# Performance work log

Measured on AMD Instinct MI355X. Metric: run time of the kernel, lower is better.

Reference implementation:

```python
import jax, jax.numpy as jnp
import numpy as np

B, T, D_IN, H, C = 256, 2048, 64, 32, 16
RHO, SPARSITY = 0.9, 0.1


def _reservoir(rng, n):
    # uniform(-1,1), scale to spectral radius RHO, then sparsify (same order as torch code)
    W = rng.uniform(-1.0, 1.0, (n, n)).astype(np.float32)
    W *= RHO / np.max(np.abs(np.linalg.eigvals(W)))
    W *= (rng.random((n, n)) < SPARSITY).astype(np.float32)
    return jnp.asarray(W)


def _linear(rng, fan_in, fan_out):
    bound = 1.0 / np.sqrt(fan_in)
    W = rng.uniform(-bound, bound, (fan_out, fan_in)).astype(np.float32)
    b = rng.uniform(-bound, bound, (fan_out,)).astype(np.float32)
    return jnp.asarray(W), jnp.asarray(b)


def setup_inputs() -> dict:
    key = jax.random.key(0)
    rng = np.random.default_rng(0)
    x = jax.random.normal(key, (B, T, D_IN), dtype=jnp.float32)
    # frozen encoder input / reservoir weights (uniform(-1,1) weights, default-init biases)
    W_in = jnp.asarray(rng.uniform(-1.0, 1.0, (H, D_IN)).astype(np.float32))
    b_in = jnp.asarray(rng.uniform(-1 / np.sqrt(D_IN), 1 / np.sqrt(D_IN), (H,)).astype(np.float32))
    W_res_enc = _reservoir(rng, H)
    b_res_enc = jnp.asarray(rng.uniform(-1 / np.sqrt(H), 1 / np.sqrt(H), (H,)).astype(np.float32))
    W_code, b_code = _linear(rng, H, C)
    W_co, b_co = _linear(rng, C, H)
    W_res_dec = _reservoir(rng, H)
    b_res_dec = jnp.asarray(rng.uniform(-1 / np.sqrt(H), 1 / np.sqrt(H), (H,)).astype(np.float32))
    W_ro, b_ro = _linear(rng, H, D_IN)
    return dict(x=x, W_in=W_in, b_in=b_in, W_res_enc=W_res_enc, b_res_enc=b_res_enc,
                W_code=W_code, b_code=b_code, W_co=W_co, b_co=b_co,
                W_res_dec=W_res_dec, b_res_dec=b_res_dec, W_ro=W_ro, b_ro=b_ro)


def reference(x, W_in, b_in, W_res_enc, b_res_enc, W_code, b_code, W_co, b_co,
              W_res_dec, b_res_dec, W_ro, b_ro):
    Bs = x.shape[0]
    h0 = jnp.zeros((Bs, W_res_enc.shape[0]), dtype=x.dtype)
    # precompute input projection for all timesteps: [T, B, H]
    u_enc = jnp.swapaxes(jnp.einsum('btd,hd->bth', x, W_in) + b_in, 0, 1)

    def enc_step(h, u):
        h = jnp.tanh(u + h @ W_res_enc.T + b_res_enc)
        return h, h

    _, enc = jax.lax.scan(enc_step, h0, u_enc)
    enc = jnp.swapaxes(enc, 0, 1)                      # [B, T, H]

    z = enc @ W_code.T + b_code                        # [B, T, C]
    h_dec_in = z @ W_co.T + b_co                       # [B, T, H]

    def dec_step(h, u):
        h = jnp.tanh(u + h @ W_res_dec.T + b_res_dec)
        return h, h

    _, dec = jax.lax.scan(dec_step, h0, jnp.swapaxes(h_dec_in, 0, 1))
    dec = jnp.swapaxes(dec, 0, 1)                      # [B, T, H]
    return dec @ W_ro.T + b_ro                         # [B, T, D_IN]
```

## Files before the change

### kernel.cpp

```cpp
#include <hip/hip_runtime.h>
#include <math.h>

#define B_    256
#define T_    2048
#define DIN   64
#define H_    32
#define C_    16

#define CHUNK 256
#define WARM  96
#define NCHUNK (T_ / CHUNK)

#define OFF_WCOMB 0u
#define OFF_BCOMB 4096u
#define OFF_U     (1u << 20)

__device__ __forceinline__ float fast_tanh(float x) {
    float e2 = __expf(x + x);
    return 1.0f - 2.0f * __builtin_amdgcn_rcpf(e2 + 1.0f);
}

__global__ __launch_bounds__(1024) void prep_kernel(
        const float* __restrict__ W_code, const float* __restrict__ b_code,
        const float* __restrict__ W_co,   const float* __restrict__ b_co,
        float* __restrict__ W_comb, float* __restrict__ b_comb) {
    int t = threadIdx.x;
    int i = t >> 5, j = t & 31;
    float s = 0.0f;
#pragma unroll
    for (int c = 0; c < C_; ++c)
        s += W_co[i * C_ + c] * W_code[c * H_ + j];
    W_comb[i * H_ + j] = s;
    if (t < H_) {
        float sb = b_co[t];
#pragma unroll
        for (int c = 0; c < C_; ++c)
            sb += W_co[t * C_ + c] * b_code[c];
        b_comb[t] = sb;
    }
}

__global__ __launch_bounds__(256) void inproj_kernel(
        const float* __restrict__ x, const float* __restrict__ W_in,
        const float* __restrict__ b_in, float* __restrict__ u) {
    __shared__ __align__(16) float4 lx[128 * 16];

    int tid  = threadIdx.x;
    int w    = tid >> 6;
    int lane = tid & 63;
    int i    = lane & 31;
    int par  = lane >> 5;

    float Wr[DIN];
    {
        const float4* wi4 = reinterpret_cast<const float4*>(W_in + i * DIN);
#pragma unroll
        for (int q = 0; q < DIN / 4; ++q) {
            float4 v = wi4[q];
            Wr[4*q+0] = v.x; Wr[4*q+1] = v.y; Wr[4*q+2] = v.z; Wr[4*q+3] = v.w;
        }
    }
    float bi = b_in[i];

    long row_base = (long)blockIdx.x * 128;
    const float4* xg = reinterpret_cast<const float4*>(x) + row_base * 16;

#pragma unroll
    for (int k = 0; k < 8; ++k)
        lx[tid + 256 * k] = xg[tid + 256 * k];
    __syncthreads();

#pragma unroll
    for (int g = 0; g < 4; ++g) {
        int r0 = w * 32 + g * 8 + par;
        float acc0 = 0.f, acc1 = 0.f, acc2 = 0.f, acc3 = 0.f;
#pragma unroll
        for (int k4 = 0; k4 < 16; ++k4) {
            float4 wv = { Wr[4*k4+0], Wr[4*k4+1], Wr[4*k4+2], Wr[4*k4+3] };
            float4 x0 = lx[(r0 + 0) * 16 + k4];
            float4 x1 = lx[(r0 + 2) * 16 + k4];
            float4 x2 = lx[(r0 + 4) * 16 + k4];
            float4 x3 = lx[(r0 + 6) * 16 + k4];
            acc0 += x0.x * wv.x + x0.y * wv.y + x0.z * wv.z + x0.w * wv.w;
            acc1 += x1.x * wv.x + x1.y * wv.y + x1.z * wv.z + x1.w * wv.w;
            acc2 += x2.x * wv.x + x2.y * wv.y + x2.z * wv.z + x2.w * wv.w;
            acc3 += x3.x * wv.x + x3.y * wv.y + x3.z * wv.z + x3.w * wv.w;
        }
        long rg = row_base + r0;
        u[(rg + 0) * H_ + i] = acc0 + bi;
        u[(rg + 2) * H_ + i] = acc1 + bi;
        u[(rg + 4) * H_ + i] = acc2 + bi;
        u[(rg + 6) * H_ + i] = acc3 + bi;
    }
}

__global__ __launch_bounds__(64, 1) void scan_kernel(
        const float* __restrict__ u,
        const float* __restrict__ W_res_enc, const float* __restrict__ b_res_enc,
        const float* __restrict__ W_res_dec, const float* __restrict__ b_res_dec,
        const float* __restrict__ W_comb,    const float* __restrict__ b_comb,
        const float* __restrict__ W_ro,      const float* __restrict__ b_ro,
        float* __restrict__ out) {
    int lane = threadIdx.x;
    int i = lane & 31;
    int half = lane >> 5;
    int b  = ((blockIdx.x & 127) << 1) | half;
    int c  = blockIdx.x >> 7;
    int t0 = c * CHUNK;
    int tstart = (c == 0) ? 0 : (t0 - WARM);
    int tend = t0 + CHUNK;

    float We[H_], Wc[H_], Wd[H_], Wo0[H_], Wo1[H_];
    {
        const float4* we4 = reinterpret_cast<const float4*>(W_res_enc + i * H_);
        const float4* wc4 = reinterpret_cast<const float4*>(W_comb + i * H_);
        const float4* wd4 = reinterpret_cast<const float4*>(W_res_dec + i * H_);
        const float4* wo0 = reinterpret_cast<const float4*>(W_ro + (2 * i) * H_);
        const float4* wo1 = reinterpret_cast<const float4*>(W_ro + (2 * i + 1) * H_);
#pragma unroll
        for (int q = 0; q < H_ / 4; ++q) {
            float4 a = we4[q], bq = wc4[q], d = wd4[q], o0 = wo0[q], o1 = wo1[q];
            We[4*q+0]=a.x;  We[4*q+1]=a.y;  We[4*q+2]=a.z;  We[4*q+3]=a.w;
            Wc[4*q+0]=bq.x; Wc[4*q+1]=bq.y; Wc[4*q+2]=bq.z; Wc[4*q+3]=bq.w;
            Wd[4*q+0]=d.x;  Wd[4*q+1]=d.y;  Wd[4*q+2]=d.z;  Wd[4*q+3]=d.w;
            Wo0[4*q+0]=o0.x;Wo0[4*q+1]=o0.y;Wo0[4*q+2]=o0.z;Wo0[4*q+3]=o0.w;
            Wo1[4*q+0]=o1.x;Wo1[4*q+1]=o1.y;Wo1[4*q+2]=o1.z;Wo1[4*q+3]=o1.w;
        }
    }
    float be = b_res_enc[i], bc = b_comb[i], bd = b_res_dec[i];
    float bo0 = b_ro[2 * i], bo1 = b_ro[2 * i + 1];

    float henc[H_], hdec[H_];
#pragma unroll
    for (int j = 0; j < H_; ++j) { henc[j] = 0.0f; hdec[j] = 0.0f; }

    __shared__ __align__(16) float lhe[2][H_];
    __shared__ __align__(16) float lhd[2][H_];

    const float* ub = u + ((long)b * T_) * H_ + i;
    float*       ob = out + ((long)b * T_) * DIN + 2 * i;

    float ucur = ub[(long)tstart * H_];
    for (int t = tstart; t < tend; ++t) {
        float unext = 0.0f;
        if (t + 1 < tend) unext = ub[(long)(t + 1) * H_];

        float a0 = ucur + be, a1 = 0.f, a2 = 0.f, a3 = 0.f;
#pragma unroll
        for (int j = 0; j < H_; j += 4) {
            a0 += We[j+0] * henc[j+0];
            a1 += We[j+1] * henc[j+1];
            a2 += We[j+2] * henc[j+2];
            a3 += We[j+3] * henc[j+3];
        }
        float a = fast_tanh((a0 + a1) + (a2 + a3));

        lhe[half][i] = a;
#pragma unroll
        for (int q = 0; q < H_ / 4; ++q) {
            float4 v = *reinterpret_cast<const float4*>(&lhe[half][4 * q]);
            henc[4*q+0] = v.x; henc[4*q+1] = v.y;
            henc[4*q+2] = v.z; henc[4*q+3] = v.w;
        }

        float g0 = bc + bd, g1 = 0.f, g2 = 0.f, g3 = 0.f;
#pragma unroll
        for (int j = 0; j < H_; j += 4) {
            g0 += Wc[j+0] * henc[j+0];
            g1 += Wc[j+1] * henc[j+1];
            g2 += Wc[j+2] * henc[j+2];
            g3 += Wc[j+3] * henc[j+3];
        }
        float d0 = 0.f, d1 = 0.f, d2 = 0.f, d3 = 0.f;
#pragma unroll
        for (int j = 0; j < H_; j += 4) {
            d0 += Wd[j+0] * hdec[j+0];
            d1 += Wd[j+1] * hdec[j+1];
            d2 += Wd[j+2] * hdec[j+2];
            d3 += Wd[j+3] * hdec[j+3];
        }
        float d = fast_tanh(((g0 + g1) + (g2 + g3)) + ((d0 + d1) + (d2 + d3)));

        lhd[half][i] = d;
#pragma unroll
        for (int q = 0; q < H_ / 4; ++q) {
            float4 v = *reinterpret_cast<const float4*>(&lhd[half][4 * q]);
            hdec[4*q+0] = v.x; hdec[4*q+1] = v.y;
            hdec[4*q+2] = v.z; hdec[4*q+3] = v.w;
        }

        if (t >= t0) {
            float s00 = bo0, s01 = 0.f, s10 = bo1, s11 = 0.f;
#pragma unroll
            for (int j = 0; j < H_; j += 2) {
                s00 += Wo0[j]     * hdec[j];
                s01 += Wo0[j + 1] * hdec[j + 1];
                s10 += Wo1[j]     * hdec[j];
                s11 += Wo1[j + 1] * hdec[j + 1];
            }
            float2 o = make_float2(s00 + s01, s10 + s11);
            *reinterpret_cast<float2*>(ob + (long)t * DIN) = o;
        }
        ucur = unext;
    }
}

extern "C" void kernel_launch(void* const* d_in, const int* in_sizes, int n_in,
                              void* d_out, int out_size, void* d_ws, size_t ws_size,
                              hipStream_t stream) {
    const float* x         = (const float*)d_in[0];
    const float* W_in      = (const float*)d_in[1];
    const float* b_in      = (const float*)d_in[2];
    const float* W_res_enc = (const float*)d_in[3];
    const float* b_res_enc = (const float*)d_in[4];
    const float* W_code    = (const float*)d_in[5];
    const float* b_code    = (const float*)d_in[6];
    const float* W_co      = (const float*)d_in[7];
    const float* b_co      = (const float*)d_in[8];
    const float* W_res_dec = (const float*)d_in[9];
    const float* b_res_dec = (const float*)d_in[10];
    const float* W_ro      = (const float*)d_in[11];
    const float* b_ro      = (const float*)d_in[12];
    float* out = (float*)d_out;

    char* ws = (char*)d_ws;
    float* W_comb = (float*)(ws + OFF_WCOMB);
    float* b_comb = (float*)(ws + OFF_BCOMB);
    float* u      = (float*)(ws + OFF_U);

    prep_kernel<<<1, 1024, 0, stream>>>(W_code, b_code, W_co, b_co, W_comb, b_comb);
    inproj_kernel<<<(B_ * T_) / 128, 256, 0, stream>>>(x, W_in, b_in, u);
    scan_kernel<<<(B_ / 2) * NCHUNK, 64, 0, stream>>>(u, W_res_enc, b_res_enc,
                                                      W_res_dec, b_res_dec,
                                                      W_comb, b_comb, W_ro, b_ro, out);
}
```

Baseline: 508.0 us.

## Split readout into separate kernel, shrink scan chunks, reorder scan step

Moves the W_ro readout out of the recurrent scan into its own GEMV kernel, so the scan writes decoder states to workspace instead of computing outputs inline. Chunk size drops to 128 with a 64-step warmup, doubling the number of scan blocks, and launch bounds now allow two blocks per CU. The loop is reordered so the decoder recurrence product overlaps the encoder LDS exchange. The input projection reads rows directly from global memory without an LDS stage. The shorter warmup risks a larger truncation error, and the extra pass over decoder states adds memory traffic.

```diff
diff --git a/kernel.cpp b/kernel.cpp
--- a/kernel.cpp
+++ b/kernel.cpp
@@ -7,13 +7,14 @@
 #define H_    32
 #define C_    16
 
-#define CHUNK 256
-#define WARM  96
+#define CHUNK 128
+#define WARM  64
 #define NCHUNK (T_ / CHUNK)
 
 #define OFF_WCOMB 0u
 #define OFF_BCOMB 4096u
 #define OFF_U     (1u << 20)
+#define OFF_DEC   ((1u << 20) + (64u << 20))
 
 __device__ __forceinline__ float fast_tanh(float x) {
     float e2 = __expf(x + x);
@@ -40,67 +41,49 @@
     }
 }
 
-__global__ __launch_bounds__(256) void inproj_kernel(
+__global__ __launch_bounds__(256, 3) void inproj_kernel(
         const float* __restrict__ x, const float* __restrict__ W_in,
         const float* __restrict__ b_in, float* __restrict__ u) {
-    __shared__ __align__(16) float4 lx[128 * 16];
-
     int tid  = threadIdx.x;
-    int w    = tid >> 6;
-    int lane = tid & 63;
-    int i    = lane & 31;
-    int par  = lane >> 5;
-
-    float Wr[DIN];
+    int wave = tid >> 6;
+    int l    = tid & 63;
+    int d    = l & 31;
+    int par  = l >> 5;
+
+    float W[DIN];
     {
-        const float4* wi4 = reinterpret_cast<const float4*>(W_in + i * DIN);
+        const float4* w4 = reinterpret_cast<const float4*>(W_in + d * DIN);
 #pragma unroll
         for (int q = 0; q < DIN / 4; ++q) {
-            float4 v = wi4[q];
-            Wr[4*q+0] = v.x; Wr[4*q+1] = v.y; Wr[4*q+2] = v.z; Wr[4*q+3] = v.w;
-        }
-    }
-    float bi = b_in[i];
-
-    long row_base = (long)blockIdx.x * 128;
-    const float4* xg = reinterpret_cast<const float4*>(x) + row_base * 16;
-
-#pragma unroll
-    for (int k = 0; k < 8; ++k)
-        lx[tid + 256 * k] = xg[tid + 256 * k];
-    __syncthreads();
-
-#pragma unroll
-    for (int g = 0; g < 4; ++g) {
-        int r0 = w * 32 + g * 8 + par;
-        float acc0 = 0.f, acc1 = 0.f, acc2 = 0.f, acc3 = 0.f;
-#pragma unroll
-        for (int k4 = 0; k4 < 16; ++k4) {
-            float4 wv = { Wr[4*k4+0], Wr[4*k4+1], Wr[4*k4+2], Wr[4*k4+3] };
-            float4 x0 = lx[(r0 + 0) * 16 + k4];
-            float4 x1 = lx[(r0 + 2) * 16 + k4];
-            float4 x2 = lx[(r0 + 4) * 16 + k4];
-            float4 x3 = lx[(r0 + 6) * 16 + k4];
-            acc0 += x0.x * wv.x + x0.y * wv.y + x0.z * wv.z + x0.w * wv.w;
-            acc1 += x1.x * wv.x + x1.y * wv.y + x1.z * wv.z + x1.w * wv.w;
-            acc2 += x2.x * wv.x + x2.y * wv.y + x2.z * wv.z + x2.w * wv.w;
-            acc3 += x3.x * wv.x + x3.y * wv.y + x3.z * wv.z + x3.w * wv.w;
-        }
-        long rg = row_base + r0;
-        u[(rg + 0) * H_ + i] = acc0 + bi;
-        u[(rg + 2) * H_ + i] = acc1 + bi;
-        u[(rg + 4) * H_ + i] = acc2 + bi;
-        u[(rg + 6) * H_ + i] = acc3 + bi;
-    }
-}
-
-__global__ __launch_bounds__(64, 1) void scan_kernel(
+            float4 v = w4[q];
+            W[4*q+0] = v.x; W[4*q+1] = v.y; W[4*q+2] = v.z; W[4*q+3] = v.w;
+        }
+    }
+    float bi = b_in[d];
+
+    long base = ((long)blockIdx.x * 4 + wave) * 64;
+    for (int it = 0; it < 32; ++it) {
+        long row = base + 2 * it + par;
+        const float4* xr = reinterpret_cast<const float4*>(x + row * DIN);
+        float a0 = bi, a1 = 0.f, a2 = 0.f, a3 = 0.f;
+#pragma unroll
+        for (int k = 0; k < DIN / 4; ++k) {
+            float4 v = xr[k];
+            a0 += v.x * W[4*k+0];
+            a1 += v.y * W[4*k+1];
+            a2 += v.z * W[4*k+2];
+            a3 += v.w * W[4*k+3];
+        }
+        u[row * H_ + d] = (a0 + a1) + (a2 + a3);
+    }
+}
+
+__global__ __launch_bounds__(64, 2) void scan_kernel(
         const float* __restrict__ u,
         const float* __restrict__ W_res_enc, const float* __restrict__ b_res_enc,
         const float* __restrict__ W_res_dec, const float* __restrict__ b_res_dec,
         const float* __restrict__ W_comb,    const float* __restrict__ b_comb,
-        const float* __restrict__ W_ro,      const float* __restrict__ b_ro,
-        float* __restrict__ out) {
+        float* __restrict__ dec) {
     int lane = threadIdx.x;
     int i = lane & 31;
     int half = lane >> 5;
@@ -110,98 +93,130 @@
     int tstart = (c == 0) ? 0 : (t0 - WARM);
     int tend = t0 + CHUNK;
 
-    float We[H_], Wc[H_], Wd[H_], Wo0[H_], Wo1[H_];
+    float We[H_], Wc[H_], Wd[H_];
     {
         const float4* we4 = reinterpret_cast<const float4*>(W_res_enc + i * H_);
         const float4* wc4 = reinterpret_cast<const float4*>(W_comb + i * H_);
         const float4* wd4 = reinterpret_cast<const float4*>(W_res_dec + i * H_);
-        const float4* wo0 = reinterpret_cast<const float4*>(W_ro + (2 * i) * H_);
-        const float4* wo1 = reinterpret_cast<const float4*>(W_ro + (2 * i + 1) * H_);
-#pragma unroll
-        for (int q = 0; q < H_ / 4; ++q) {
-            float4 a = we4[q], bq = wc4[q], d = wd4[q], o0 = wo0[q], o1 = wo1[q];
+#pragma unroll
+        for (int q = 0; q < H_ / 4; ++q) {
+            float4 a = we4[q], bq = wc4[q], dv = wd4[q];
             We[4*q+0]=a.x;  We[4*q+1]=a.y;  We[4*q+2]=a.z;  We[4*q+3]=a.w;
             Wc[4*q+0]=bq.x; Wc[4*q+1]=bq.y; Wc[4*q+2]=bq.z; Wc[4*q+3]=bq.w;
-            Wd[4*q+0]=d.x;  Wd[4*q+1]=d.y;  Wd[4*q+2]=d.z;  Wd[4*q+3]=d.w;
-            Wo0[4*q+0]=o0.x;Wo0[4*q+1]=o0.y;Wo0[4*q+2]=o0.z;Wo0[4*q+3]=o0.w;
-            Wo1[4*q+0]=o1.x;Wo1[4*q+1]=o1.y;Wo1[4*q+2]=o1.z;Wo1[4*q+3]=o1.w;
-        }
-    }
-    float be = b_res_enc[i], bc = b_comb[i], bd = b_res_dec[i];
-    float bo0 = b_ro[2 * i], bo1 = b_ro[2 * i + 1];
-
-    float henc[H_], hdec[H_];
-#pragma unroll
-    for (int j = 0; j < H_; ++j) { henc[j] = 0.0f; hdec[j] = 0.0f; }
+            Wd[4*q+0]=dv.x; Wd[4*q+1]=dv.y; Wd[4*q+2]=dv.z; Wd[4*q+3]=dv.w;
+        }
+    }
+    float be = b_res_enc[i];
+    float bcd = b_comb[i] + b_res_dec[i];
+
+    float he[H_], hd[H_];
+#pragma unroll
+    for (int j = 0; j < H_; ++j) { he[j] = 0.0f; hd[j] = 0.0f; }
 
     __shared__ __align__(16) float lhe[2][H_];
     __shared__ __align__(16) float lhd[2][H_];
 
     const float* ub = u + ((long)b * T_) * H_ + i;
-    float*       ob = out + ((long)b * T_) * DIN + 2 * i;
+    float*       db = dec + ((long)b * T_) * H_ + i;
+
+    float4 hdr[H_ / 4];
+#pragma unroll
+    for (int q = 0; q < H_ / 4; ++q) hdr[q] = make_float4(0.f, 0.f, 0.f, 0.f);
 
     float ucur = ub[(long)tstart * H_];
     for (int t = tstart; t < tend; ++t) {
+        float a0 = ucur + be, a1 = 0.f, a2 = 0.f, a3 = 0.f;
+#pragma unroll
+        for (int j = 0; j < H_; j += 4) {
+            a0 += We[j+0] * he[j+0];
+            a1 += We[j+1] * he[j+1];
+            a2 += We[j+2] * he[j+2];
+            a3 += We[j+3] * he[j+3];
+        }
+        float a = fast_tanh((a0 + a1) + (a2 + a3));
+
+        lhe[half][i] = a;
+        float4 her[H_ / 4];
+#pragma unroll
+        for (int q = 0; q < H_ / 4; ++q)
+            her[q] = *reinterpret_cast<const float4*>(&lhe[half][4 * q]);
+
+#pragma unroll
+        for (int q = 0; q < H_ / 4; ++q) {
+            hd[4*q+0] = hdr[q].x; hd[4*q+1] = hdr[q].y;
+            hd[4*q+2] = hdr[q].z; hd[4*q+3] = hdr[q].w;
+        }
+        float d0 = bcd, d1 = 0.f, d2 = 0.f, d3 = 0.f;
+#pragma unroll
+        for (int j = 0; j < H_; j += 4) {
+            d0 += Wd[j+0] * hd[j+0];
+            d1 += Wd[j+1] * hd[j+1];
+            d2 += Wd[j+2] * hd[j+2];
+            d3 += Wd[j+3] * hd[j+3];
+        }
+
         float unext = 0.0f;
         if (t + 1 < tend) unext = ub[(long)(t + 1) * H_];
 
-        float a0 = ucur + be, a1 = 0.f, a2 = 0.f, a3 = 0.f;
+#pragma unroll
+        for (int q = 0; q < H_ / 4; ++q) {
+            he[4*q+0] = her[q].x; he[4*q+1] = her[q].y;
+            he[4*q+2] = her[q].z; he[4*q+3] = her[q].w;
+        }
+
+        float g0 = 0.f, g1 = 0.f, g2 = 0.f, g3 = 0.f;
 #pragma unroll
         for (int j = 0; j < H_; j += 4) {
-            a0 += We[j+0] * henc[j+0];
-            a1 += We[j+1] * henc[j+1];
-            a2 += We[j+2] * henc[j+2];
-            a3 += We[j+3] * henc[j+3];
-        }
-        float a = fast_tanh((a0 + a1) + (a2 + a3));
-
-        lhe[half][i] = a;
-#pragma unroll
-        for (int q = 0; q < H_ / 4; ++q) {
-            float4 v = *reinterpret_cast<const float4*>(&lhe[half][4 * q]);
-            henc[4*q+0] = v.x; henc[4*q+1] = v.y;
-            henc[4*q+2] = v.z; henc[4*q+3] = v.w;
-        }
-
-        float g0 = bc + bd, g1 = 0.f, g2 = 0.f, g3 = 0.f;
-#pragma unroll
-        for (int j = 0; j < H_; j += 4) {
-            g0 += Wc[j+0] * henc[j+0];
-            g1 += Wc[j+1] * henc[j+1];
-            g2 += Wc[j+2] * henc[j+2];
-            g3 += Wc[j+3] * henc[j+3];
-        }
-        float d0 = 0.f, d1 = 0.f, d2 = 0.f, d3 = 0.f;
-#pragma unroll
-        for (int j = 0; j < H_; j += 4) {
-            d0 += Wd[j+0] * hdec[j+0];
-            d1 += Wd[j+1] * hdec[j+1];
-            d2 += Wd[j+2] * hdec[j+2];
-            d3 += Wd[j+3] * hdec[j+3];
+            g0 += Wc[j+0] * he[j+0];
+            g1 += Wc[j+1] * he[j+1];
+            g2 += Wc[j+2] * he[j+2];
+            g3 += Wc[j+3] * he[j+3];
         }
         float d = fast_tanh(((g0 + g1) + (g2 + g3)) + ((d0 + d1) + (d2 + d3)));
 
+        if (t >= t0) db[(long)t * H_] = d;
+
         lhd[half][i] = d;
 #pragma unroll
-        for (int q = 0; q < H_ / 4; ++q) {
-            float4 v = *reinterpret_cast<const float4*>(&lhd[half][4 * q]);
-            hdec[4*q+0] = v.x; hdec[4*q+1] = v.y;
-            hdec[4*q+2] = v.z; hdec[4*q+3] = v.w;
-        }
-
-        if (t >= t0) {
-            float s00 = bo0, s01 = 0.f, s10 = bo1, s11 = 0.f;
-#pragma unroll
-            for (int j = 0; j < H_; j += 2) {
-                s00 += Wo0[j]     * hdec[j];
-                s01 += Wo0[j + 1] * hdec[j + 1];
-                s10 += Wo1[j]     * hdec[j];
-                s11 += Wo1[j + 1] * hdec[j + 1];
-            }
-            float2 o = make_float2(s00 + s01, s10 + s11);
-            *reinterpret_cast<float2*>(ob + (long)t * DIN) = o;
-        }
+        for (int q = 0; q < H_ / 4; ++q)
+            hdr[q] = *reinterpret_cast<const float4*>(&lhd[half][4 * q]);
+
         ucur = unext;
+    }
+}
+
+__global__ __launch_bounds__(256, 3) void readout_kernel(
+        const float* __restrict__ dec, const float* __restrict__ W_ro,
+        const float* __restrict__ b_ro, float* __restrict__ out) {
+    int tid  = threadIdx.x;
+    int wave = tid >> 6;
+    int l    = tid & 63;
+
+    float W[H_];
+    {
+        const float4* w4 = reinterpret_cast<const float4*>(W_ro + l * H_);
+#pragma unroll
+        for (int q = 0; q < H_ / 4; ++q) {
+            float4 v = w4[q];
+            W[4*q+0] = v.x; W[4*q+1] = v.y; W[4*q+2] = v.z; W[4*q+3] = v.w;
+        }
+    }
+    float bo = b_ro[l];
+
+    long base = ((long)blockIdx.x * 4 + wave) * 64;
+    for (int it = 0; it < 64; ++it) {
+        long r = base + it;
+        const float4* dr = reinterpret_cast<const float4*>(dec + r * H_);
+        float a0 = bo, a1 = 0.f, a2 = 0.f, a3 = 0.f;
+#pragma unroll
+        for (int q = 0; q < H_ / 4; ++q) {
+            float4 v = dr[q];
+            a0 += v.x * W[4*q+0];
+            a1 += v.y * W[4*q+1];
+            a2 += v.z * W[4*q+2];
+            a3 += v.w * W[4*q+3];
+        }
+        out[r * DIN + l] = (a0 + a1) + (a2 + a3);
     }
 }
 
@@ -227,10 +242,12 @@
     float* W_comb = (float*)(ws + OFF_WCOMB);
     float* b_comb = (float*)(ws + OFF_BCOMB);
     float* u      = (float*)(ws + OFF_U);
+    float* decs   = (float*)(ws + OFF_DEC);
 
     prep_kernel<<<1, 1024, 0, stream>>>(W_code, b_code, W_co, b_co, W_comb, b_comb);
-    inproj_kernel<<<(B_ * T_) / 128, 256, 0, stream>>>(x, W_in, b_in, u);
+    inproj_kernel<<<(B_ * T_) / 256, 256, 0, stream>>>(x, W_in, b_in, u);
     scan_kernel<<<(B_ / 2) * NCHUNK, 64, 0, stream>>>(u, W_res_enc, b_res_enc,
                                                       W_res_dec, b_res_dec,
-                                                      W_comb, b_comb, W_ro, b_ro, out);
-}
+                                                      W_comb, b_comb, decs);
+    readout_kernel<<<(B_ * T_) / 256, 256, 0, stream>>>(decs, W_ro, b_ro, out);
+}
```

New measurement: 729.9 us. 43.7% more time.
